# Kernel optimization log

Measured on AMD Instinct MI355X. Metric: run time of the kernel, lower is better.

The kernel has to match this reference:

```python
import jax, jax.numpy as jnp
import numpy as np

GROUP = 64          # quantization group size along input dim
EPS = 1e-6          # rms_norm_eps
THETA = 1000000.0   # rope theta
NUM_HEADS = 16
NUM_KV_HEADS = 4
HEAD_DIM = 128


def _qlinear(x, wq, s, b=None):
    # dequantize int8-valued weights with per-group scales, then GEMM
    o, i = wq.shape
    w = (wq.reshape(o, i // GROUP, GROUP).astype(jnp.float32) * s[:, :, None]).reshape(o, i)
    y = jnp.einsum('bsi,oi->bso', x, w)
    return y + b if b is not None else y


def _rmsnorm(x, w):
    return x * jax.lax.rsqrt(jnp.mean(x * x, axis=-1, keepdims=True) + EPS) * w


def _rope(x, offset):
    # x: [B, H, S, hd], neox-style half rotation
    hd = x.shape[-1]
    S = x.shape[2]
    pos = (jnp.arange(S) + offset).astype(jnp.float32)
    inv = THETA ** (-(jnp.arange(0, hd, 2).astype(jnp.float32)) / hd)  # [hd/2]
    ang = pos[:, None] * inv[None, :]                                  # [S, hd/2]
    cos, sin = jnp.cos(ang), jnp.sin(ang)
    x1, x2 = x[..., : hd // 2], x[..., hd // 2 :]
    return jnp.concatenate([x1 * cos - x2 * sin, x2 * cos + x1 * sin], axis=-1)


def setup_inputs() -> dict:
    key = jax.random.key(0)
    B, S, D, I = 2, 1024, 2048, 5632
    KV = NUM_KV_HEADS * HEAD_DIM  # 512
    keys = iter(jax.random.split(key, 32))

    def qw(shape):
        return jax.random.randint(next(keys), shape, -127, 128, dtype=jnp.int32)

    def sc(shape):
        return jax.random.uniform(next(keys), shape, jnp.float32, 0.5, 1.5) * 0.001

    inp = {
        'x': jax.random.normal(next(keys), (B, S, D), jnp.float32),
        'wq_q': qw((D, D)),   'wq_s': sc((D, D // GROUP)),
        'bq': jax.random.normal(next(keys), (D,), jnp.float32) * 0.02,
        'wk_q': qw((KV, D)),  'wk_s': sc((KV, D // GROUP)),
        'bk': jax.random.normal(next(keys), (KV,), jnp.float32) * 0.02,
        'wv_q': qw((KV, D)),  'wv_s': sc((KV, D // GROUP)),
        'bv': jax.random.normal(next(keys), (KV,), jnp.float32) * 0.02,
        'wo_q': qw((D, D)),   'wo_s': sc((D, D // GROUP)),
        'gate_q': qw((I, D)), 'gate_s': sc((I, D // GROUP)),
        'up_q': qw((I, D)),   'up_s': sc((I, D // GROUP)),
        'down_q': qw((D, I)), 'down_s': sc((D, I // GROUP)),
        'w_in_ln': jnp.ones((D,), jnp.float32),
        'w_post_ln': jnp.ones((D,), jnp.float32),
        'offset': 0,
    }
    return inp


def reference(x, wq_q, wq_s, bq, wk_q, wk_s, bk, wv_q, wv_s, bv, wo_q, wo_s,
              gate_q, gate_s, up_q, up_s, down_q, down_s, w_in_ln, w_post_ln, offset):
    B, S, D = x.shape
    H, KVH, hd = NUM_HEADS, NUM_KV_HEADS, HEAD_DIM

    # --- attention sub-block ---
    h = _rmsnorm(x, w_in_ln)
    q = _qlinear(h, wq_q, wq_s, bq).reshape(B, S, H, hd).transpose(0, 2, 1, 3)
    k = _qlinear(h, wk_q, wk_s, bk).reshape(B, S, KVH, hd).transpose(0, 2, 1, 3)
    v = _qlinear(h, wv_q, wv_s, bv).reshape(B, S, KVH, hd).transpose(0, 2, 1, 3)
    q = _rope(q, offset)
    k = _rope(k, offset)

    g = H // KVH  # query groups per kv head
    qg = q.reshape(B, KVH, g, S, hd)
    scores = jnp.einsum('bghsd,bgtd->bghst', qg, k) * (1.0 / np.sqrt(hd)).astype(np.float32)
    causal = jnp.tril(jnp.ones((S, S), dtype=bool))  # prefill causal mask (empty cache)
    scores = jnp.where(causal, scores, jnp.float32(-1e9))
    p = jax.nn.softmax(scores, axis=-1)
    o = jnp.einsum('bghst,bgtd->bghsd', p, v)
    o = o.reshape(B, H, S, hd).transpose(0, 2, 1, 3).reshape(B, S, D)
    x = x + _qlinear(o, wo_q, wo_s)

    # --- mlp sub-block ---
    h2 = _rmsnorm(x, w_post_ln)
    gate = jax.nn.silu(_qlinear(h2, gate_q, gate_s))
    up = _qlinear(h2, up_q, up_s)
    mlp = _qlinear(gate * up, down_q, down_s)
    return x + mlp
```

## Files before the change

### kernel.cpp

```cpp
#include <hip/hip_runtime.h>
#include <cstdint>
#include <cstddef>

#define DEV __device__ __forceinline__

typedef _Float16 f16x8 __attribute__((ext_vector_type(8)));
typedef float f32x4 __attribute__((ext_vector_type(4)));

static constexpr int D_MODEL = 2048;
static constexpr int D_FF    = 5632;
static constexpr int N_QKV   = 3072;
static constexpr int SEQ     = 1024;
static constexpr int BATCH   = 2;
static constexpr int ROWS    = BATCH * SEQ;
static constexpr int HEADS   = 16;
static constexpr int HD      = 128;

DEV uint16_t f2h(float f) {
    return __builtin_bit_cast(uint16_t, (_Float16)f);
}

DEV void async_load16(const void* g, void* lds) {
    __builtin_amdgcn_global_load_lds(
        reinterpret_cast<__attribute__((address_space(1))) void*>(
            reinterpret_cast<uintptr_t>(g)),
        reinterpret_cast<__attribute__((address_space(3))) void*>(
            static_cast<uint32_t>(reinterpret_cast<uintptr_t>(lds))),
        16, 0, 0);
}

static constexpr int DQ_BLOCKS = 44032;

__global__ __launch_bounds__(256)
void dequant_all_kernel(const int* __restrict__ wq_q, const float* __restrict__ wq_s,
                        const int* __restrict__ wk_q, const float* __restrict__ wk_s,
                        const int* __restrict__ wv_q, const float* __restrict__ wv_s,
                        const int* __restrict__ wo_q, const float* __restrict__ wo_s,
                        const int* __restrict__ gate_q, const float* __restrict__ gate_s,
                        const int* __restrict__ up_q, const float* __restrict__ up_s,
                        const int* __restrict__ down_q, const float* __restrict__ down_s,
                        uint16_t* __restrict__ Wqkv, uint16_t* __restrict__ Wo,
                        uint16_t* __restrict__ Wgu, uint16_t* __restrict__ Wdown)
{
    const int bid = blockIdx.x;
    const int* q; const float* s; uint16_t* out; int I, mode, seg0;
    if (bid < 4096)        { q = wq_q;   s = wq_s;   out = Wqkv;                      I = 2048; mode = 0; seg0 = 0; }
    else if (bid < 5120)   { q = wk_q;   s = wk_s;   out = Wqkv + 2048 * 2048;        I = 2048; mode = 0; seg0 = 4096; }
    else if (bid < 6144)   { q = wv_q;   s = wv_s;   out = Wqkv + 2560 * 2048;        I = 2048; mode = 0; seg0 = 5120; }
    else if (bid < 10240)  { q = wo_q;   s = wo_s;   out = Wo;                        I = 2048; mode = 0; seg0 = 6144; }
    else if (bid < 21504)  { q = gate_q; s = gate_s; out = Wgu;                       I = 2048; mode = 1; seg0 = 10240; }
    else if (bid < 32768)  { q = up_q;   s = up_s;   out = Wgu;                       I = 2048; mode = 2; seg0 = 21504; }
    else                   { q = down_q; s = down_s; out = Wdown;                     I = 5632; mode = 0; seg0 = 32768; }

    const int idx = (bid - seg0) * 256 + threadIdx.x;
    const int e = idx * 4;
    const int row = e / I;
    const int i = e - row * I;
    const int4 qv = *reinterpret_cast<const int4*>(&q[e]);
    const float scf = s[row * (I >> 6) + (i >> 6)];
    int orow = row;
    if (mode == 1) orow = ((row >> 4) << 5) + (row & 15);
    else if (mode == 2) orow = ((row >> 4) << 5) + (row & 15) + 16;
    uint16_t h[4];
    h[0] = f2h((float)qv.x * scf);
    h[1] = f2h((float)qv.y * scf);
    h[2] = f2h((float)qv.z * scf);
    h[3] = f2h((float)qv.w * scf);
    uint2 pk;
    pk.x = (uint32_t)h[0] | ((uint32_t)h[1] << 16);
    pk.y = (uint32_t)h[2] | ((uint32_t)h[3] << 16);
    *reinterpret_cast<uint2*>(&out[(size_t)orow * I + i]) = pk;
}

__global__ __launch_bounds__(256)
void rmsnorm_kernel(const float* __restrict__ x, const float* __restrict__ wln,
                    uint16_t* __restrict__ out)
{
    __shared__ float red[4];
    const int row = blockIdx.x;
    const int tid = threadIdx.x;
    const float* xr = x + (size_t)row * D_MODEL;
    const float4 v0 = *reinterpret_cast<const float4*>(&xr[tid * 8]);
    const float4 v1 = *reinterpret_cast<const float4*>(&xr[tid * 8 + 4]);
    float ss = v0.x*v0.x + v0.y*v0.y + v0.z*v0.z + v0.w*v0.w
             + v1.x*v1.x + v1.y*v1.y + v1.z*v1.z + v1.w*v1.w;
#pragma unroll
    for (int off = 32; off; off >>= 1) ss += __shfl_xor(ss, off);
    if ((tid & 63) == 0) red[tid >> 6] = ss;
    __syncthreads();
    const float rms = rsqrtf((red[0] + red[1] + red[2] + red[3]) * (1.0f / D_MODEL) + 1e-6f);
    const int cb = tid * 8;
    const size_t base = (size_t)row * D_MODEL + cb;
    const float vals[8] = {v0.x, v0.y, v0.z, v0.w, v1.x, v1.y, v1.z, v1.w};
#pragma unroll
    for (int k = 0; k < 8; k += 2) {
        const uint16_t h0 = f2h(vals[k] * rms * wln[cb + k]);
        const uint16_t h1 = f2h(vals[k + 1] * rms * wln[cb + k + 1]);
        *reinterpret_cast<uint32_t*>(&out[base + k]) = (uint32_t)h0 | ((uint32_t)h1 << 16);
    }
}

DEV void xcd_remap(int bid, int nwg, int nBm, int& bm, int& bn) {
    const int cpx = nwg >> 3;
    const int wg  = (bid & 7) * cpx + (bid >> 3);
    bm = wg % nBm;
    bn = wg / nBm;
}

__global__ __launch_bounds__(256)
void gemm_f16_glu_kernel(const uint16_t* __restrict__ A, const uint16_t* __restrict__ W,
                         uint16_t* __restrict__ outh, int M, int N, int K)
{
    __shared__ uint16_t sA[2][128 * 64];
    __shared__ uint16_t sB[2][128 * 64];

    const int tid  = threadIdx.x;
    const int lane = tid & 63;
    const int wv   = tid >> 6;
    const int wm   = wv >> 1;
    const int wn   = wv & 1;
    const int quad = lane >> 4;
    const int l16  = lane & 15;

    int bm, bn;
    xcd_remap(blockIdx.x, gridDim.x, M >> 7, bm, bn);
    const int m0  = bm << 7;
    const int n0  = bn << 7;

    f32x4 acc[4][4];
#pragma unroll
    for (int i = 0; i < 4; i++)
#pragma unroll
        for (int j = 0; j < 4; j++)
            acc[i][j] = (f32x4){0.f, 0.f, 0.f, 0.f};

    const uint16_t* Ab = A + (size_t)m0 * K;
    const uint16_t* Wb = W + (size_t)n0 * K;

    auto stage = [&](int kt, int bsel) {
#pragma unroll
        for (int p = 0; p < 4; p++) {
            const int cb = p * 256 + wv * 64;
            const int c  = cb + lane;
            const int row = c >> 3;
            const int g   = (c & 7) ^ (row & 7);
            const size_t goff = (size_t)row * K + kt + g * 8;
            async_load16(Ab + goff, &sA[bsel][cb * 8]);
            async_load16(Wb + goff, &sB[bsel][cb * 8]);
        }
    };

    stage(0, 0);
    __syncthreads();

    const int nKt = K >> 6;
    for (int t = 0; t < nKt; t++) {
        const int cur = t & 1;
        if (t + 1 < nKt) stage((t + 1) << 6, cur ^ 1);
        const uint16_t* sAc = sA[cur];
        const uint16_t* sBc = sB[cur];
#pragma unroll
        for (int kk = 0; kk < 2; kk++) {
            const int gsw = ((kk * 4 + quad) ^ (l16 & 7)) * 8;
            f16x8 bfv[4];
#pragma unroll
            for (int j = 0; j < 4; j++)
                bfv[j] = *reinterpret_cast<const f16x8*>(
                    &sBc[(wn * 64 + j * 16 + l16) * 64 + gsw]);
#pragma unroll
            for (int i = 0; i < 4; i++) {
                const f16x8 af = *reinterpret_cast<const f16x8*>(
                    &sAc[(wm * 64 + i * 16 + l16) * 64 + gsw]);
#pragma unroll
                for (int j = 0; j < 4; j++)
                    acc[i][j] = __builtin_amdgcn_mfma_f32_16x16x32_f16(af, bfv[j], acc[i][j], 0, 0, 0);
            }
        }
        __syncthreads();
    }

    const int NH = N >> 1;
#pragma unroll
    for (int i = 0; i < 4; i++) {
        const int rowb = m0 + wm * 64 + i * 16 + quad * 4;
#pragma unroll
        for (int r = 0; r < 4; r++) {
            const size_t rr = (size_t)(rowb + r);
#pragma unroll
            for (int pjt = 0; pjt < 2; pjt++) {
                const float g = acc[i][2 * pjt][r];
                const float u = acc[i][2 * pjt + 1][r];
                const float a = (g / (1.0f + __expf(-g))) * u;
                const int cc = (n0 >> 1) + wn * 32 + pjt * 16 + l16;
                outh[rr * NH + cc] = f2h(a);
            }
        }
    }
}

__global__ __launch_bounds__(256)
void gemm_f16_m64_kernel(const uint16_t* __restrict__ A, const uint16_t* __restrict__ W,
                         const float* __restrict__ bq, const float* __restrict__ bk,
                         const float* __restrict__ bv, const float* __restrict__ resid,
                         float* __restrict__ outf, int M, int N, int K)
{
    __shared__ uint16_t sA[2][64 * 64];
    __shared__ uint16_t sB[2][128 * 64];

    const int tid  = threadIdx.x;
    const int lane = tid & 63;
    const int wv   = tid >> 6;
    const int quad = lane >> 4;
    const int l16  = lane & 15;

    int bm, bn;
    xcd_remap(blockIdx.x, gridDim.x, M >> 6, bm, bn);
    const int m0  = bm << 6;
    const int n0  = bn << 7;

    f32x4 acc[4][2];
#pragma unroll
    for (int i = 0; i < 4; i++)
#pragma unroll
        for (int j = 0; j < 2; j++)
            acc[i][j] = (f32x4){0.f, 0.f, 0.f, 0.f};

    const uint16_t* Ab = A + (size_t)m0 * K;
    const uint16_t* Wb = W + (size_t)n0 * K;

    auto stage = [&](int kt, int bsel) {
#pragma unroll
        for (int p = 0; p < 2; p++) {
            const int cb = p * 256 + wv * 64;
            const int c  = cb + lane;
            const int row = c >> 3;
            const int g   = (c & 7) ^ (row & 7);
            async_load16(Ab + (size_t)row * K + kt + g * 8, &sA[bsel][cb * 8]);
        }
#pragma unroll
        for (int p = 0; p < 4; p++) {
            const int cb = p * 256 + wv * 64;
            const int c  = cb + lane;
            const int row = c >> 3;
            const int g   = (c & 7) ^ (row & 7);
            async_load16(Wb + (size_t)row * K + kt + g * 8, &sB[bsel][cb * 8]);
        }
    };

    stage(0, 0);
    __syncthreads();

    const int nKt = K >> 6;
    for (int t = 0; t < nKt; t++) {
        const int cur = t & 1;
        if (t + 1 < nKt) stage((t + 1) << 6, cur ^ 1);
        const uint16_t* sAc = sA[cur];
        const uint16_t* sBc = sB[cur];
#pragma unroll
        for (int kk = 0; kk < 2; kk++) {
            const int gsw = ((kk * 4 + quad) ^ (l16 & 7)) * 8;
            f16x8 bfv[2];
#pragma unroll
            for (int j = 0; j < 2; j++)
                bfv[j] = *reinterpret_cast<const f16x8*>(
                    &sBc[(wv * 32 + j * 16 + l16) * 64 + gsw]);
#pragma unroll
            for (int i = 0; i < 4; i++) {
                const f16x8 af = *reinterpret_cast<const f16x8*>(
                    &sAc[(i * 16 + l16) * 64 + gsw]);
#pragma unroll
                for (int j = 0; j < 2; j++)
                    acc[i][j] = __builtin_amdgcn_mfma_f32_16x16x32_f16(af, bfv[j], acc[i][j], 0, 0, 0);
            }
        }
        __syncthreads();
    }

#pragma unroll
    for (int i = 0; i < 4; i++) {
        const int rowb = m0 + i * 16 + quad * 4;
#pragma unroll
        for (int r = 0; r < 4; r++) {
            const size_t rr = (size_t)(rowb + r);
#pragma unroll
            for (int j = 0; j < 2; j++) {
                const int cc = n0 + wv * 32 + j * 16 + l16;
                float v = acc[i][j][r];
                if (bq) {
                    float bb;
                    if (cc < 2048)      bb = bq[cc];
                    else if (cc < 2560) bb = bk[cc - 2048];
                    else                bb = bv[cc - 2560];
                    v += bb;
                }
                if (resid) v += resid[rr * N + cc];
                outf[rr * N + cc] = v;
            }
        }
    }
}

static constexpr int ROPE_Q_THREADS = ROWS * 16 * 64;
static constexpr int ROPE_THREADS   = ROPE_Q_THREADS + ROWS * 4 * 64;

__global__ __launch_bounds__(256)
void rope_qk_kernel(const float* __restrict__ qkv, const int* __restrict__ offp,
                    uint16_t* __restrict__ Qb, uint16_t* __restrict__ Kb)
{
    const int gidx = blockIdx.x * 256 + threadIdx.x;
    if (gidx < ROPE_Q_THREADS) {
        const int idx = gidx;
        const int d   = idx & 63;
        const int h   = (idx >> 6) & 15;
        const int row = idx >> 10;
        const int b   = row >> 10;
        const int s   = row & (SEQ - 1);
        const float pos  = (float)(s + *offp);
        const float freq = powf(1.0e6f, -(float)d * (1.0f / 64.0f));
        float sn, cs;
        sincosf(pos * freq, &sn, &cs);
        const size_t gb = (size_t)row * N_QKV + h * HD + d;
        const float x1 = qkv[gb];
        const float x2 = qkv[gb + 64];
        const float qscale = 0.08838834764831845f;
        const size_t ob = ((size_t)(b * 16 + h) * SEQ + s) * HD + d;
        Qb[ob]      = f2h((x1 * cs - x2 * sn) * qscale);
        Qb[ob + 64] = f2h((x2 * cs + x1 * sn) * qscale);
    } else {
        const int idx = gidx - ROPE_Q_THREADS;
        const int d   = idx & 63;
        const int kvh = (idx >> 6) & 3;
        const int row = idx >> 8;
        const int b   = row >> 10;
        const int s   = row & (SEQ - 1);
        const float pos  = (float)(s + *offp);
        const float freq = powf(1.0e6f, -(float)d * (1.0f / 64.0f));
        float sn, cs;
        sincosf(pos * freq, &sn, &cs);
        const size_t gb = (size_t)row * N_QKV + 2048 + kvh * HD + d;
        const float x1 = qkv[gb];
        const float x2 = qkv[gb + 64];
        const size_t ob = ((size_t)(b * 4 + kvh) * SEQ + s) * HD + d;
        Kb[ob]      = f2h(x1 * cs - x2 * sn);
        Kb[ob + 64] = f2h(x2 * cs + x1 * sn);
    }
}

__global__ __launch_bounds__(256)
void prep_v_kernel(const float* __restrict__ qkv, uint16_t* __restrict__ Vt)
{
    __shared__ uint16_t sh[128 * 72];
    const int tid = threadIdx.x;
    const int sc  = blockIdx.x & 15;
    const int bk  = blockIdx.x >> 4;
    const int b   = bk >> 2, kvh = bk & 3;
#pragma unroll
    for (int p = 0; p < 8; p++) {
        const int q4 = p * 256 + tid;
        const int sloc = q4 >> 5, d4 = (q4 & 31) * 4;
        const float4 v = *reinterpret_cast<const float4*>(
            &qkv[(size_t)(b * SEQ + sc * 64 + sloc) * N_QKV + 2560 + kvh * HD + d4]);
        sh[(d4 + 0) * 72 + sloc] = f2h(v.x);
        sh[(d4 + 1) * 72 + sloc] = f2h(v.y);
        sh[(d4 + 2) * 72 + sloc] = f2h(v.z);
        sh[(d4 + 3) * 72 + sloc] = f2h(v.w);
    }
    __syncthreads();
    const int d = tid >> 1, half = tid & 1;
    const size_t ob = ((size_t)(bk * 128 + d)) * SEQ + sc * 64 + half * 32;
    const uint16_t* srh = &sh[d * 72 + half * 32];
#pragma unroll
    for (int k = 0; k < 4; k++)
        *reinterpret_cast<uint4*>(&Vt[ob + k * 8]) =
            *reinterpret_cast<const uint4*>(&srh[k * 8]);
}

__global__ __launch_bounds__(256)
void attn_kernel(const uint16_t* __restrict__ Qb, const uint16_t* __restrict__ Kb,
                 const uint16_t* __restrict__ Vt, uint16_t* __restrict__ att)
{
    __shared__ uint16_t sK[2][32 * 128];
    __shared__ uint16_t sV[2][128 * 32];
    __shared__ uint16_t sP[4 * 16 * 32];

    const int tid  = threadIdx.x;
    const int lane = tid & 63;
    const int wv   = tid >> 6;
    const int quad = lane >> 4;
    const int l16  = lane & 15;
    const int qsw  = (quad ^ ((l16 >> 1) & 3)) * 8;

    const int bi  = blockIdx.x;
    const int sc  = 15 - (bi >> 5);
    const int bh  = bi & 31;
    const int b   = bh >> 4;
    const int h   = bh & 15;
    const int kvh = h >> 2;
    const int s0  = sc << 6;

    f16x8 qf[4];
    {
        const size_t qb = ((size_t)(b * 16 + h) * SEQ + s0 + wv * 16 + l16) * HD;
#pragma unroll
        for (int ks = 0; ks < 4; ks++)
            qf[ks] = *reinterpret_cast<const f16x8*>(&Qb[qb + ks * 32 + quad * 8]);
    }

    float m_i[4], l_i[4];
#pragma unroll
    for (int r = 0; r < 4; r++) { m_i[r] = -1e30f; l_i[r] = 0.f; }
    f32x4 oacc[8];
#pragma unroll
    for (int dt = 0; dt < 8; dt++) oacc[dt] = (f32x4){0.f, 0.f, 0.f, 0.f};

    const size_t kb = (size_t)(b * 4 + kvh) * SEQ * HD;
    const size_t vb = (size_t)(b * 4 + kvh) * HD * SEQ;

    auto stageKV = [&](int t0, int bsel) {
#pragma unroll
        for (int p = 0; p < 2; p++) {
            const int cb = p * 256 + wv * 64;
            const int c  = cb + lane;
            const int krow = c >> 4;
            const int kcc  = (c & 15) ^ (krow & 7);
            async_load16(Kb + kb + (size_t)(t0 + krow) * HD + kcc * 8, &sK[bsel][cb * 8]);
            const int vrow = c >> 2;
            const int vcc  = (c & 3) ^ ((vrow >> 1) & 3);
            async_load16(Vt + vb + (size_t)vrow * SEQ + t0 + vcc * 8, &sV[bsel][cb * 8]);
        }
    };

    const int ntiles = 2 * sc + 2;
    stageKV(0, 0);
    __syncthreads();

    for (int tt = 0; tt < ntiles; tt++) {
        const int t0 = tt << 5;
        const int cur = tt & 1;
        if (tt + 1 < ntiles) stageKV((tt + 1) << 5, cur ^ 1);

        f32x4 sacc[2];
        sacc[0] = (f32x4){0.f, 0.f, 0.f, 0.f};
        sacc[1] = (f32x4){0.f, 0.f, 0.f, 0.f};
#pragma unroll
        for (int ks = 0; ks < 4; ks++) {
#pragma unroll
            for (int jt = 0; jt < 2; jt++) {
                const int idx = (jt * 16 + l16) * 128 + (((ks * 4 + quad) ^ (l16 & 7)) * 8);
                const f16x8 kf = *reinterpret_cast<const f16x8*>(&sK[cur][idx]);
                sacc[jt] = __builtin_amdgcn_mfma_f32_16x16x32_f16(qf[ks], kf, sacc[jt], 0, 0, 0);
            }
        }

        if (t0 >= s0) {
            const int rowg = s0 + wv * 16 + quad * 4;
#pragma unroll
            for (int jt = 0; jt < 2; jt++) {
                const int key = t0 + jt * 16 + l16;
#pragma unroll
                for (int r = 0; r < 4; r++)
                    if (key > rowg + r) sacc[jt][r] = -1e30f;
            }
        }

        float alpha[4];
#pragma unroll
        for (int r = 0; r < 4; r++) {
            float mt = fmaxf(sacc[0][r], sacc[1][r]);
#pragma unroll
            for (int off = 8; off; off >>= 1) mt = fmaxf(mt, __shfl_xor(mt, off));
            const float mn = fmaxf(m_i[r], mt);
            alpha[r] = __expf(m_i[r] - mn);
            const float p0 = __expf(sacc[0][r] - mn);
            const float p1 = __expf(sacc[1][r] - mn);
            float ps = p0 + p1;
#pragma unroll
            for (int off = 8; off; off >>= 1) ps += __shfl_xor(ps, off);
            l_i[r] = l_i[r] * alpha[r] + ps;
            m_i[r] = mn;
            const int prow = quad * 4 + r;
            sP[wv * 512 + prow * 32 + 0 * 16 + l16] = f2h(p0);
            sP[wv * 512 + prow * 32 + 1 * 16 + l16] = f2h(p1);
        }

#pragma unroll
        for (int dt = 0; dt < 8; dt++) {
#pragma unroll
            for (int r = 0; r < 4; r++) oacc[dt][r] *= alpha[r];
        }
        const f16x8 pf = *reinterpret_cast<const f16x8*>(&sP[wv * 512 + l16 * 32 + quad * 8]);
#pragma unroll
        for (int dt = 0; dt < 8; dt++) {
            const f16x8 vf = *reinterpret_cast<const f16x8*>(&sV[cur][(dt * 16 + l16) * 32 + qsw]);
            oacc[dt] = __builtin_amdgcn_mfma_f32_16x16x32_f16(pf, vf, oacc[dt], 0, 0, 0);
        }

        __syncthreads();
    }

    float inv[4];
#pragma unroll
    for (int r = 0; r < 4; r++) inv[r] = 1.0f / l_i[r];
#pragma unroll
    for (int r = 0; r < 4; r++) {
        const size_t rowg = (size_t)(b * SEQ + s0 + wv * 16 + quad * 4 + r);
#pragma unroll
        for (int dt = 0; dt < 8; dt++)
            att[rowg * D_MODEL + h * HD + dt * 16 + l16] = f2h(oacc[dt][r] * inv[r]);
    }
}

extern "C" void kernel_launch(void* const* d_in, const int* in_sizes, int n_in,
                              void* d_out, int out_size, void* d_ws, size_t ws_size,
                              hipStream_t stream)
{
    (void)in_sizes; (void)n_in; (void)out_size; (void)ws_size;
    const float* x      = (const float*)d_in[0];
    const int*   wq_q   = (const int*)d_in[1];
    const float* wq_s   = (const float*)d_in[2];
    const float* bq     = (const float*)d_in[3];
    const int*   wk_q   = (const int*)d_in[4];
    const float* wk_s   = (const float*)d_in[5];
    const float* bk     = (const float*)d_in[6];
    const int*   wv_q   = (const int*)d_in[7];
    const float* wv_s   = (const float*)d_in[8];
    const float* bv     = (const float*)d_in[9];
    const int*   wo_q   = (const int*)d_in[10];
    const float* wo_s   = (const float*)d_in[11];
    const int*   gate_q = (const int*)d_in[12];
    const float* gate_s = (const float*)d_in[13];
    const int*   up_q   = (const int*)d_in[14];
    const float* up_s   = (const float*)d_in[15];
    const int*   down_q = (const int*)d_in[16];
    const float* down_s = (const float*)d_in[17];
    const float* w_in   = (const float*)d_in[18];
    const float* w_post = (const float*)d_in[19];
    const int*   offp   = (const int*)d_in[20];

    char* p = (char*)d_ws;
    auto alloc = [&](size_t bytes) {
        char* r = p;
        p += (bytes + 255) & ~(size_t)255;
        return r;
    };
    uint16_t* Wgu   = (uint16_t*)alloc((size_t)2 * D_FF * D_MODEL * 2);
    uint16_t* Wdown = (uint16_t*)alloc((size_t)D_MODEL * D_FF * 2);
    uint16_t* hbuf  = (uint16_t*)alloc((size_t)ROWS * D_MODEL * 2);
    float*    x2    = (float*)alloc((size_t)ROWS * D_MODEL * 4);
    char* zone = alloc((size_t)N_QKV * D_MODEL * 2 +
                       (size_t)D_MODEL * D_MODEL * 2 +
                       (size_t)ROWS * N_QKV * 4 + 8192);
    uint16_t* Wqkv = (uint16_t*)zone;
    uint16_t* Wo   = Wqkv + (size_t)N_QKV * D_MODEL;
    float*    qkv  = (float*)(Wo + (size_t)D_MODEL * D_MODEL);
    uint16_t* Qb = Wqkv;
    uint16_t* Kb = Qb + (size_t)BATCH * 16 * SEQ * HD;
    uint16_t* Vt = Kb + (size_t)BATCH * 4 * SEQ * HD;
    uint16_t* att = (uint16_t*)qkv;
    uint16_t* act = (uint16_t*)zone;

    dequant_all_kernel<<<DQ_BLOCKS, 256, 0, stream>>>(
        wq_q, wq_s, wk_q, wk_s, wv_q, wv_s, wo_q, wo_s,
        gate_q, gate_s, up_q, up_s, down_q, down_s,
        Wqkv, Wo, Wgu, Wdown);

    rmsnorm_kernel<<<ROWS, 256, 0, stream>>>(x, w_in, hbuf);

    gemm_f16_m64_kernel<<<(ROWS / 64) * (N_QKV / 128), 256, 0, stream>>>(
        hbuf, Wqkv, bq, bk, bv, nullptr, qkv, ROWS, N_QKV, D_MODEL);

    rope_qk_kernel<<<ROPE_THREADS / 256, 256, 0, stream>>>(qkv, offp, Qb, Kb);
    prep_v_kernel<<<BATCH * 4 * (SEQ / 64), 256, 0, stream>>>(qkv, Vt);

    attn_kernel<<<BATCH * HEADS * (SEQ / 64), 256, 0, stream>>>(Qb, Kb, Vt, att);

    gemm_f16_m64_kernel<<<(ROWS / 64) * (D_MODEL / 128), 256, 0, stream>>>(
        att, Wo, nullptr, nullptr, nullptr, x, x2, ROWS, D_MODEL, D_MODEL);

    rmsnorm_kernel<<<ROWS, 256, 0, stream>>>(x2, w_post, hbuf);

    gemm_f16_glu_kernel<<<(ROWS / 128) * (2 * D_FF / 128), 256, 0, stream>>>(
        hbuf, Wgu, act, ROWS, 2 * D_FF, D_MODEL);

    gemm_f16_m64_kernel<<<(ROWS / 64) * (D_MODEL / 128), 256, 0, stream>>>(
        act, Wdown, nullptr, nullptr, nullptr, x2, (float*)d_out, ROWS, D_MODEL, D_FF);
}
```

Baseline: 558.3 us.

## Switch output GEMMs to 128x128 tiles and drop XCD block remapping

Replaces the 64x128 GEMM kernel with a 128x128 tile version using a 2x2 wave layout, giving each wave a 64x64 sub-tile with more MFMA per LDS load. It also removes the XCD-aware block remapping in both GEMM kernels and uses plain row-major block indexing instead. Larger tiles cut global and LDS traffic per flop but halve the grid size. For the N=2048 GEMMs that means only 256 blocks, so the 256 CUs are filled just once and any tail hurts. Dropping the remap may lower L2 locality across XCDs.

```diff
diff --git a/kernel.cpp b/kernel.cpp
--- a/kernel.cpp
+++ b/kernel.cpp
@@ -100,13 +100,6 @@
     }
 }
 
-DEV void xcd_remap(int bid, int nwg, int nBm, int& bm, int& bn) {
-    const int cpx = nwg >> 3;
-    const int wg  = (bid & 7) * cpx + (bid >> 3);
-    bm = wg % nBm;
-    bn = wg / nBm;
-}
-
 __global__ __launch_bounds__(256)
 void gemm_f16_glu_kernel(const uint16_t* __restrict__ A, const uint16_t* __restrict__ W,
                          uint16_t* __restrict__ outh, int M, int N, int K)
@@ -122,8 +115,9 @@
     const int quad = lane >> 4;
     const int l16  = lane & 15;
 
-    int bm, bn;
-    xcd_remap(blockIdx.x, gridDim.x, M >> 7, bm, bn);
+    const int nBn = N >> 7;
+    const int bm  = blockIdx.x / nBn;
+    const int bn  = blockIdx.x - bm * nBn;
     const int m0  = bm << 7;
     const int n0  = bn << 7;
 
@@ -199,51 +193,48 @@
 }
 
 __global__ __launch_bounds__(256)
-void gemm_f16_m64_kernel(const uint16_t* __restrict__ A, const uint16_t* __restrict__ W,
-                         const float* __restrict__ bq, const float* __restrict__ bk,
-                         const float* __restrict__ bv, const float* __restrict__ resid,
-                         float* __restrict__ outf, int M, int N, int K)
-{
-    __shared__ uint16_t sA[2][64 * 64];
+void gemm_f16_m128_kernel(const uint16_t* __restrict__ A, const uint16_t* __restrict__ W,
+                          const float* __restrict__ bq, const float* __restrict__ bk,
+                          const float* __restrict__ bv, const float* __restrict__ resid,
+                          float* __restrict__ outf, int M, int N, int K)
+{
+    __shared__ uint16_t sA[2][128 * 64];
     __shared__ uint16_t sB[2][128 * 64];
 
     const int tid  = threadIdx.x;
     const int lane = tid & 63;
     const int wv   = tid >> 6;
+    const int wm   = wv >> 1;
+    const int wn   = wv & 1;
     const int quad = lane >> 4;
     const int l16  = lane & 15;
 
-    int bm, bn;
-    xcd_remap(blockIdx.x, gridDim.x, M >> 6, bm, bn);
-    const int m0  = bm << 6;
+    const int nBn = N >> 7;
+    const int bm  = blockIdx.x / nBn;
+    const int bn  = blockIdx.x - bm * nBn;
+    const int m0  = bm << 7;
     const int n0  = bn << 7;
 
-    f32x4 acc[4][2];
+    f32x4 acc[4][4];
 #pragma unroll
     for (int i = 0; i < 4; i++)
 #pragma unroll
-        for (int j = 0; j < 2; j++)
+        for (int j = 0; j < 4; j++)
             acc[i][j] = (f32x4){0.f, 0.f, 0.f, 0.f};
 
     const uint16_t* Ab = A + (size_t)m0 * K;
     const uint16_t* Wb = W + (size_t)n0 * K;
 
     auto stage = [&](int kt, int bsel) {
-#pragma unroll
-        for (int p = 0; p < 2; p++) {
-            const int cb = p * 256 + wv * 64;
-            const int c  = cb + lane;
-            const int row = c >> 3;
-            const int g   = (c & 7) ^ (row & 7);
-            async_load16(Ab + (size_t)row * K + kt + g * 8, &sA[bsel][cb * 8]);
-        }
 #pragma unroll
         for (int p = 0; p < 4; p++) {
             const int cb = p * 256 + wv * 64;
             const int c  = cb + lane;
             const int row = c >> 3;
             const int g   = (c & 7) ^ (row & 7);
-            async_load16(Wb + (size_t)row * K + kt + g * 8, &sB[bsel][cb * 8]);
+            const size_t goff = (size_t)row * K + kt + g * 8;
+            async_load16(Ab + goff, &sA[bsel][cb * 8]);
+            async_load16(Wb + goff, &sB[bsel][cb * 8]);
         }
     };
 
@@ -259,17 +250,17 @@
 #pragma unroll
         for (int kk = 0; kk < 2; kk++) {
             const int gsw = ((kk * 4 + quad) ^ (l16 & 7)) * 8;
-            f16x8 bfv[2];
-#pragma unroll
-            for (int j = 0; j < 2; j++)
+            f16x8 bfv[4];
+#pragma unroll
+            for (int j = 0; j < 4; j++)
                 bfv[j] = *reinterpret_cast<const f16x8*>(
-                    &sBc[(wv * 32 + j * 16 + l16) * 64 + gsw]);
+                    &sBc[(wn * 64 + j * 16 + l16) * 64 + gsw]);
 #pragma unroll
             for (int i = 0; i < 4; i++) {
                 const f16x8 af = *reinterpret_cast<const f16x8*>(
-                    &sAc[(i * 16 + l16) * 64 + gsw]);
-#pragma unroll
-                for (int j = 0; j < 2; j++)
+                    &sAc[(wm * 64 + i * 16 + l16) * 64 + gsw]);
+#pragma unroll
+                for (int j = 0; j < 4; j++)
                     acc[i][j] = __builtin_amdgcn_mfma_f32_16x16x32_f16(af, bfv[j], acc[i][j], 0, 0, 0);
             }
         }
@@ -278,13 +269,13 @@
 
 #pragma unroll
     for (int i = 0; i < 4; i++) {
-        const int rowb = m0 + i * 16 + quad * 4;
+        const int rowb = m0 + wm * 64 + i * 16 + quad * 4;
 #pragma unroll
         for (int r = 0; r < 4; r++) {
             const size_t rr = (size_t)(rowb + r);
 #pragma unroll
-            for (int j = 0; j < 2; j++) {
-                const int cc = n0 + wv * 32 + j * 16 + l16;
+            for (int j = 0; j < 4; j++) {
+                const int cc = n0 + wn * 64 + j * 16 + l16;
                 float v = acc[i][j][r];
                 if (bq) {
                     float bb;
@@ -566,7 +557,7 @@
 
     rmsnorm_kernel<<<ROWS, 256, 0, stream>>>(x, w_in, hbuf);
 
-    gemm_f16_m64_kernel<<<(ROWS / 64) * (N_QKV / 128), 256, 0, stream>>>(
+    gemm_f16_m128_kernel<<<(ROWS / 128) * (N_QKV / 128), 256, 0, stream>>>(
         hbuf, Wqkv, bq, bk, bv, nullptr, qkv, ROWS, N_QKV, D_MODEL);
 
     rope_qk_kernel<<<ROPE_THREADS / 256, 256, 0, stream>>>(qkv, offp, Qb, Kb);
@@ -574,7 +565,7 @@
 
     attn_kernel<<<BATCH * HEADS * (SEQ / 64), 256, 0, stream>>>(Qb, Kb, Vt, att);
 
-    gemm_f16_m64_kernel<<<(ROWS / 64) * (D_MODEL / 128), 256, 0, stream>>>(
+    gemm_f16_m128_kernel<<<(ROWS / 128) * (D_MODEL / 128), 256, 0, stream>>>(
         att, Wo, nullptr, nullptr, nullptr, x, x2, ROWS, D_MODEL, D_MODEL);
 
     rmsnorm_kernel<<<ROWS, 256, 0, stream>>>(x2, w_post, hbuf);
@@ -582,6 +573,6 @@
     gemm_f16_glu_kernel<<<(ROWS / 128) * (2 * D_FF / 128), 256, 0, stream>>>(
         hbuf, Wgu, act, ROWS, 2 * D_FF, D_MODEL);
 
-    gemm_f16_m64_kernel<<<(ROWS / 64) * (D_MODEL / 128), 256, 0, stream>>>(
+    gemm_f16_m128_kernel<<<(ROWS / 128) * (D_MODEL / 128), 256, 0, stream>>>(
         act, Wdown, nullptr, nullptr, nullptr, x2, (float*)d_out, ROWS, D_MODEL, D_FF);
 }
```

Result: no change. 563.8 us (+1.0%).
